# Optimization experiments

Hardware: AMD Instinct MI355X
Metric: run time of the kernel (lower is better)

Reference implementation:

```python
import jax, jax.numpy as jnp
import numpy as np

N = 100000
F_IN = 128
F_OUT = 128
NNZ = 1_600_000  # avg degree 16


def spmm(rows, cols, vals, X, n):
    """Sparse [n,n] (COO: rows, cols, vals) times dense X [n,d] -> [n,d]."""
    return jax.ops.segment_sum(vals[:, None] * X[cols], rows, num_segments=n)


def setup_inputs() -> dict:
    key = jax.random.key(0)
    ks = jax.random.split(key, 8)
    x = jax.random.normal(ks[0], (N, F_IN), dtype=jnp.float32)
    W = jax.random.normal(ks[1], (F_IN, F_OUT), dtype=jnp.float32) * 0.05
    kernel = jnp.ones((N, 1), dtype=jnp.float32)  # tf.ones_initializer
    phi0_rows = jax.random.randint(ks[2], (NNZ,), 0, N, dtype=jnp.int64)
    phi0_cols = jax.random.randint(ks[3], (NNZ,), 0, N, dtype=jnp.int64)
    phi0_vals = jax.random.uniform(ks[4], (NNZ,), dtype=jnp.float32)
    phi1_rows = jax.random.randint(ks[5], (NNZ,), 0, N, dtype=jnp.int64)
    phi1_cols = jax.random.randint(ks[6], (NNZ,), 0, N, dtype=jnp.int64)
    phi1_vals = jax.random.uniform(ks[7], (NNZ,), dtype=jnp.float32)
    return {
        "x": x, "W": W, "kernel": kernel,
        "phi0_rows": phi0_rows, "phi0_cols": phi0_cols, "phi0_vals": phi0_vals,
        "phi1_rows": phi1_rows, "phi1_cols": phi1_cols, "phi1_vals": phi1_vals,
    }


def reference(x, W, kernel, phi0_rows, phi0_cols, phi0_vals,
              phi1_rows, phi1_cols, phi1_vals):
    # X' = x @ W  (dense feature projection)
    X_prime = x @ W  # [N, F_OUT]
    # X'_t = phi0 @ X'  (SpMM with wavelet basis)
    X_t = spmm(phi0_rows, phi0_cols, phi0_vals, X_prime, N)
    # out = phi1 @ (kernel * X'_t)  (elementwise spectral scaling then SpMM)
    out = spmm(phi1_rows, phi1_cols, phi1_vals, kernel * X_t, N)
    return jax.nn.relu(out)
```

## Files before the change

### kernel.cpp

```cpp
#include <hip/hip_runtime.h>


constexpr int kN = 100000;
constexpr int kF = 128;
constexpr int kNNZ = 1600000;

constexpr int kBuckets = (kN + 255) / 256;
constexpr int kBucketCap = 4608;
constexpr int kChunk = 7168;
constexpr int kChunkBlocks = (kNNZ + kChunk - 1) / kChunk;
constexpr int kSlotsPerMat = kChunkBlocks * kChunk;
constexpr int kDirStride = kBuckets + 1;
constexpr int kGemmBlocks = (kN + 63) / 64;
constexpr int kRowBlocks = kN * 32 / 256;
constexpr int kTransBlocks = 64;

typedef short bf16x8 __attribute__((ext_vector_type(8)));
typedef float f32x4 __attribute__((ext_vector_type(4)));
typedef unsigned short ushort4v __attribute__((ext_vector_type(4)));

__device__ __forceinline__ unsigned short f32_to_bf16(float f) {
    unsigned int u = __float_as_uint(f);
    u += 0x7fffu + ((u >> 16) & 1u);
    return (unsigned short)(u >> 16);
}
__device__ __forceinline__ float bf16_to_f32(unsigned short h) {
    return __uint_as_float((unsigned int)h << 16);
}

__global__ __launch_bounds__(256) void scatter_transpose(
    const float* __restrict__ W, unsigned short* __restrict__ Wt,
    const int* __restrict__ r0, const int* __restrict__ c0, const float* __restrict__ v0,
    const int* __restrict__ r1, const int* __restrict__ c1, const float* __restrict__ v1,
    unsigned long long* __restrict__ stg, unsigned short* __restrict__ dir) {
    const int t = threadIdx.x;
    if (blockIdx.x < kTransBlocks) {
        const int e = blockIdx.x * 256 + t;
        const int n = e & 127, k = e >> 7;
        Wt[n * 128 + k] = f32_to_bf16(W[e]);
        return;
    }

    __shared__ unsigned long long recs[kChunk];
    __shared__ int hist[kDirStride];
    __shared__ int cur[kDirStride];
    __shared__ int sc2[256];

    const int b = blockIdx.x - kTransBlocks;
    const bool m1 = b >= kChunkBlocks;
    const int cb = m1 ? b - kChunkBlocks : b;
    const int* rows = m1 ? r1 : r0;
    const int* cols = m1 ? c1 : c0;
    const float* vals = m1 ? v1 : v0;
    unsigned long long* dst = stg + (size_t)b * kChunk;
    unsigned short* dirm = dir + (size_t)b * kDirStride;

    for (int i = t; i < kDirStride; i += 256) hist[i] = 0;
    __syncthreads();

    const int base0 = cb * kChunk;
    const int cnt = min(kNNZ - base0, kChunk);

    for (int j = t; j < cnt; j += 256) atomicAdd(&hist[rows[base0 + j] >> 8], 1);
    __syncthreads();

    int s = 0;
    if (t < 196) s = hist[2 * t] + hist[2 * t + 1];
    sc2[t] = (t < 196) ? s : 0;
    __syncthreads();
    #pragma unroll
    for (int off = 1; off < 256; off <<= 1) {
        const int add = (t >= off) ? sc2[t - off] : 0;
        __syncthreads();
        sc2[t] += add;
        __syncthreads();
    }
    if (t < 196) {
        const int ex = sc2[t] - s;
        cur[2 * t] = ex;
        cur[2 * t + 1] = ex + hist[2 * t];
        dirm[2 * t] = (unsigned short)ex;
        dirm[2 * t + 1] = (unsigned short)(ex + hist[2 * t]);
    }
    __syncthreads();

    for (int j = t; j < cnt; j += 256) {
        const int idx = base0 + j;
        const int r = rows[idx];
        const int bk = r >> 8;
        const int pos = atomicAdd(&cur[bk], 1);
        const unsigned int key = ((unsigned int)(r & 255) << 17) | (unsigned int)cols[idx];
        recs[pos] = ((unsigned long long)__float_as_uint(vals[idx]) << 32) | key;
    }
    __syncthreads();

    for (int j = t; j < cnt; j += 256) dst[j] = recs[j];
}

__global__ __launch_bounds__(256) void gemm_mfma(const float* __restrict__ x,
                                                 const unsigned short* __restrict__ Wt,
                                                 unsigned short* __restrict__ Xpb) {
    __shared__ __align__(16) unsigned short xs[64 * 128];
    const int t = threadIdx.x;
    const int rowBase = blockIdx.x * 64;

    {
        const int lrow = t >> 2;
        const int q = t & 3;
        int srow = rowBase + lrow;
        if (srow >= kN) srow = kN - 1;
        const float4* xr = (const float4*)(x + (size_t)srow * kF) + q * 8;
        #pragma unroll
        for (int i = 0; i < 8; ++i) {
            const float4 f = xr[i];
            ushort4v h;
            h.x = f32_to_bf16(f.x); h.y = f32_to_bf16(f.y);
            h.z = f32_to_bf16(f.z); h.w = f32_to_bf16(f.w);
            const int kidx = q * 32 + i * 4;
            *(ushort4v*)&xs[lrow * 128 + (kidx ^ ((lrow & 7) << 3))] = h;
        }
    }
    __syncthreads();

    const int w = t >> 6;
    const int l = t & 63;
    const int lr = l & 15;
    const int lq = l >> 4;

    f32x4 acc[8];
    #pragma unroll
    for (int n = 0; n < 8; ++n) acc[n] = (f32x4){0.f, 0.f, 0.f, 0.f};

    const int arow = w * 16 + lr;
    #pragma unroll
    for (int ks = 0; ks < 4; ++ks) {
        const int akidx = ks * 32 + lq * 8;
        const bf16x8 a = *(const bf16x8*)&xs[arow * 128 + (akidx ^ ((arow & 7) << 3))];
        #pragma unroll
        for (int n = 0; n < 8; ++n) {
            const int bn = n * 16 + lr;
            const bf16x8 b = *(const bf16x8*)(Wt + bn * 128 + akidx);
            acc[n] = __builtin_amdgcn_mfma_f32_16x16x32_bf16(a, b, acc[n], 0, 0, 0);
        }
    }

    #pragma unroll
    for (int j = 0; j < 4; ++j) {
        const int row = rowBase + w * 16 + lq * 4 + j;
        if (row < kN) {
            unsigned short* orow = Xpb + (size_t)row * kF + lr;
            #pragma unroll
            for (int n = 0; n < 8; ++n) orow[n * 16] = f32_to_bf16(acc[n][j]);
        }
    }
}

__global__ __launch_bounds__(512) void bucket_sort(
    const unsigned long long* __restrict__ stg,
    const unsigned short* __restrict__ dir,
    unsigned long long* __restrict__ sortedG,
    int* __restrict__ rs, int* __restrict__ re) {
    __shared__ unsigned long long sorted[kBucketCap];
    __shared__ int rlen[kChunkBlocks];
    __shared__ int gst[kChunkBlocks];
    __shared__ int hist[256];
    __shared__ int sc[256];
    __shared__ int cur[256];

    const int bidx = blockIdx.x;
    const bool m1 = bidx >= kBuckets;
    const int bk = m1 ? bidx - kBuckets : bidx;
    const int t = threadIdx.x;
    const unsigned long long* stgm = stg + (m1 ? (size_t)kSlotsPerMat : 0);

    if (t < kChunkBlocks) {
        const unsigned short* dd =
            dir + (size_t)((m1 ? kChunkBlocks : 0) + t) * kDirStride;
        const int s = dd[bk];
        rlen[t] = dd[bk + 1] - s;
        gst[t] = t * kChunk + s;
    }
    if (t < 256) hist[t] = 0;
    __syncthreads();

    const int g = t >> 5;
    const int lane = t & 31;

    for (int blk = g; blk < kChunkBlocks; blk += 16) {
        const int len = rlen[blk];
        const int gs = gst[blk];
        for (int i = lane; i < len; i += 32) {
            const unsigned int lo = (unsigned int)stgm[gs + i];
            atomicAdd(&hist[(lo >> 17) & 255], 1);
        }
    }
    __syncthreads();

    const int v = (t < 256) ? hist[t] : 0;
    if (t < 256) sc[t] = v;
    __syncthreads();
    #pragma unroll
    for (int off = 1; off < 256; off <<= 1) {
        const int add = (t < 256 && t >= off) ? sc[t - off] : 0;
        __syncthreads();
        if (t < 256) sc[t] += add;
        __syncthreads();
    }
    if (t < 256) cur[t] = sc[t] - v;
    __syncthreads();

    for (int blk = g; blk < kChunkBlocks; blk += 16) {
        const int len = rlen[blk];
        const int gs = gst[blk];
        for (int i = lane; i < len; i += 32) {
            const unsigned long long p = stgm[gs + i];
            const int lrow = (int)(((unsigned int)p >> 17) & 255);
            sorted[atomicAdd(&cur[lrow], 1)] = p;
        }
    }
    __syncthreads();

    const int nrec = sc[255];
    const size_t outBase = (size_t)bidx * kBucketCap;
    for (int j = t; j < nrec; j += 512) sortedG[outBase + j] = sorted[j];
    if (t < 256) {
        const int row = bk * 256 + t;
        if (row < kN) {
            const int rg = (m1 ? kN : 0) + row;
            rs[rg] = (int)outBase + sc[t] - hist[t];
            re[rg] = (int)outBase + sc[t];
        }
    }
}

template <bool ROW_SCALE, bool RELU, bool OUT_BF16>
__global__ __launch_bounds__(256) void spmm_csr(const int* __restrict__ rs,
                                                const int* __restrict__ re,
                                                const unsigned long long* __restrict__ rec,
                                                const float* __restrict__ scale,
                                                const unsigned short* __restrict__ Xin,
                                                void* __restrict__ Xout) {
    const int tid = blockIdx.x * 256 + threadIdx.x;
    const int r = tid >> 5;
    const int lane = tid & 31;

    const int s = rs[r];
    const int e = re[r];

    float4 acc = make_float4(0.f, 0.f, 0.f, 0.f);

    for (int base = s; base < e; base += 32) {
        int cl = 0;
        float vl = 0.f;
        if (base + lane < e) {
            const unsigned long long p = rec[base + lane];
            cl = (int)((unsigned int)p & 0x1FFFF);
            vl = __uint_as_float((unsigned int)(p >> 32));
        }
        const int m4 = (min(32, e - base) + 3) & ~3;
        for (int j = 0; j < m4; j += 4) {
            const int c0 = __shfl(cl, j, 32);
            const int c1 = __shfl(cl, j + 1, 32);
            const int c2 = __shfl(cl, j + 2, 32);
            const int c3 = __shfl(cl, j + 3, 32);
            const float w0 = __shfl(vl, j, 32);
            const float w1 = __shfl(vl, j + 1, 32);
            const float w2 = __shfl(vl, j + 2, 32);
            const float w3 = __shfl(vl, j + 3, 32);
            const ushort4v x0 = *(const ushort4v*)(Xin + (size_t)c0 * kF + lane * 4);
            const ushort4v x1 = *(const ushort4v*)(Xin + (size_t)c1 * kF + lane * 4);
            const ushort4v x2 = *(const ushort4v*)(Xin + (size_t)c2 * kF + lane * 4);
            const ushort4v x3 = *(const ushort4v*)(Xin + (size_t)c3 * kF + lane * 4);
            acc.x = fmaf(w0, bf16_to_f32(x0.x), acc.x);
            acc.y = fmaf(w0, bf16_to_f32(x0.y), acc.y);
            acc.z = fmaf(w0, bf16_to_f32(x0.z), acc.z);
            acc.w = fmaf(w0, bf16_to_f32(x0.w), acc.w);
            acc.x = fmaf(w1, bf16_to_f32(x1.x), acc.x);
            acc.y = fmaf(w1, bf16_to_f32(x1.y), acc.y);
            acc.z = fmaf(w1, bf16_to_f32(x1.z), acc.z);
            acc.w = fmaf(w1, bf16_to_f32(x1.w), acc.w);
            acc.x = fmaf(w2, bf16_to_f32(x2.x), acc.x);
            acc.y = fmaf(w2, bf16_to_f32(x2.y), acc.y);
            acc.z = fmaf(w2, bf16_to_f32(x2.z), acc.z);
            acc.w = fmaf(w2, bf16_to_f32(x2.w), acc.w);
            acc.x = fmaf(w3, bf16_to_f32(x3.x), acc.x);
            acc.y = fmaf(w3, bf16_to_f32(x3.y), acc.y);
            acc.z = fmaf(w3, bf16_to_f32(x3.z), acc.z);
            acc.w = fmaf(w3, bf16_to_f32(x3.w), acc.w);
        }
    }
    if (ROW_SCALE) {
        const float k = scale[r];
        acc.x *= k; acc.y *= k; acc.z *= k; acc.w *= k;
    }
    if (RELU) {
        acc.x = fmaxf(acc.x, 0.f); acc.y = fmaxf(acc.y, 0.f);
        acc.z = fmaxf(acc.z, 0.f); acc.w = fmaxf(acc.w, 0.f);
    }
    if (OUT_BF16) {
        ushort4v o;
        o.x = f32_to_bf16(acc.x); o.y = f32_to_bf16(acc.y);
        o.z = f32_to_bf16(acc.z); o.w = f32_to_bf16(acc.w);
        *(ushort4v*)((unsigned short*)Xout + (size_t)r * kF + lane * 4) = o;
    } else {
        ((float4*)Xout)[(size_t)r * 32 + lane] = acc;
    }
}

extern "C" void kernel_launch(void* const* d_in, const int* in_sizes, int n_in,
                              void* d_out, int out_size, void* d_ws, size_t ws_size,
                              hipStream_t stream) {
    const float* x    = (const float*)d_in[0];
    const float* W    = (const float*)d_in[1];
    const float* kern = (const float*)d_in[2];
    const int*   p0r  = (const int*)d_in[3];
    const int*   p0c  = (const int*)d_in[4];
    const float* p0v  = (const float*)d_in[5];
    const int*   p1r  = (const int*)d_in[6];
    const int*   p1c  = (const int*)d_in[7];
    const float* p1v  = (const float*)d_in[8];

    unsigned long long* stg = (unsigned long long*)d_out;

    char* w = (char*)d_ws;
    size_t off = 0;
    unsigned short* Xpb = (unsigned short*)(w + off); off += (size_t)kN * kF * 2;
    unsigned short* Xtb = (unsigned short*)(w + off); off += (size_t)kN * kF * 2;
    unsigned short* Wt = (unsigned short*)(w + off);  off += 128 * 128 * 2;
    unsigned short* dir = (unsigned short*)(w + off);
    off += (size_t)2 * kChunkBlocks * kDirStride * 2;
    off = (off + 15) & ~(size_t)15;
    unsigned long long* sortedG = (unsigned long long*)(w + off);
    off += (size_t)2 * kBuckets * kBucketCap * 8;
    int* rs = (int*)(w + off);                        off += (size_t)2 * kN * 4;
    int* re = (int*)(w + off);                        off += (size_t)2 * kN * 4;

    scatter_transpose<<<kTransBlocks + 2 * kChunkBlocks, 256, 0, stream>>>(
        W, Wt, p0r, p0c, p0v, p1r, p1c, p1v, stg, dir);

    gemm_mfma<<<kGemmBlocks, 256, 0, stream>>>(x, Wt, Xpb);

    bucket_sort<<<2 * kBuckets, 512, 0, stream>>>(stg, dir, sortedG, rs, re);

    spmm_csr<true, false, true><<<kRowBlocks, 256, 0, stream>>>(
        rs, re, sortedG, kern, Xpb, Xtb);

    spmm_csr<false, true, false><<<kRowBlocks, 256, 0, stream>>>(
        rs + kN, re + kN, sortedG, nullptr, Xtb, (float*)d_out);
}
```

Before: 214.2 us.

## Merge bucket sort and GEMM into one launch; use nontemporal loads/stores in SpMM

Combines the bucket_sort and gemm_mfma kernels into one launch. Blocks branch by index to do either sorting or a GEMM over a 128-row tile with 512 threads, so the two independent stages can overlap on the GPU and one launch gap goes away. The SpMM kernel now uses nontemporal loads for the edge records and nontemporal stores for its outputs, to avoid polluting the cache that holds the gathered feature rows. The costs are a larger shared-memory footprint per block (a union of both layouts), which may lower occupancy for the GEMM blocks. The nontemporal output of the first SpMM may also hurt reuse when the second SpMM reads it.

```diff
diff --git a/kernel.cpp b/kernel.cpp
--- a/kernel.cpp
+++ b/kernel.cpp
@@ -11,9 +11,10 @@
 constexpr int kChunkBlocks = (kNNZ + kChunk - 1) / kChunk;
 constexpr int kSlotsPerMat = kChunkBlocks * kChunk;
 constexpr int kDirStride = kBuckets + 1;
-constexpr int kGemmBlocks = (kN + 63) / 64;
+constexpr int kTransBlocks = 64;
+constexpr int kSortBlocks = 2 * kBuckets;
+constexpr int kGemmBlocks = (kN + 127) / 128;
 constexpr int kRowBlocks = kN * 32 / 256;
-constexpr int kTransBlocks = 64;
 
 typedef short bf16x8 __attribute__((ext_vector_type(8)));
 typedef float f32x4 __attribute__((ext_vector_type(4)));
@@ -97,138 +98,139 @@
     for (int j = t; j < cnt; j += 256) dst[j] = recs[j];
 }
 
-__global__ __launch_bounds__(256) void gemm_mfma(const float* __restrict__ x,
-                                                 const unsigned short* __restrict__ Wt,
-                                                 unsigned short* __restrict__ Xpb) {
-    __shared__ __align__(16) unsigned short xs[64 * 128];
-    const int t = threadIdx.x;
-    const int rowBase = blockIdx.x * 64;
-
-    {
-        const int lrow = t >> 2;
-        const int q = t & 3;
-        int srow = rowBase + lrow;
-        if (srow >= kN) srow = kN - 1;
-        const float4* xr = (const float4*)(x + (size_t)srow * kF) + q * 8;
-        #pragma unroll
-        for (int i = 0; i < 8; ++i) {
-            const float4 f = xr[i];
-            ushort4v h;
-            h.x = f32_to_bf16(f.x); h.y = f32_to_bf16(f.y);
-            h.z = f32_to_bf16(f.z); h.w = f32_to_bf16(f.w);
-            const int kidx = q * 32 + i * 4;
-            *(ushort4v*)&xs[lrow * 128 + (kidx ^ ((lrow & 7) << 3))] = h;
-        }
-    }
-    __syncthreads();
-
-    const int w = t >> 6;
-    const int l = t & 63;
-    const int lr = l & 15;
-    const int lq = l >> 4;
-
-    f32x4 acc[8];
-    #pragma unroll
-    for (int n = 0; n < 8; ++n) acc[n] = (f32x4){0.f, 0.f, 0.f, 0.f};
-
-    const int arow = w * 16 + lr;
-    #pragma unroll
-    for (int ks = 0; ks < 4; ++ks) {
-        const int akidx = ks * 32 + lq * 8;
-        const bf16x8 a = *(const bf16x8*)&xs[arow * 128 + (akidx ^ ((arow & 7) << 3))];
-        #pragma unroll
-        for (int n = 0; n < 8; ++n) {
-            const int bn = n * 16 + lr;
-            const bf16x8 b = *(const bf16x8*)(Wt + bn * 128 + akidx);
-            acc[n] = __builtin_amdgcn_mfma_f32_16x16x32_bf16(a, b, acc[n], 0, 0, 0);
-        }
-    }
-
-    #pragma unroll
-    for (int j = 0; j < 4; ++j) {
-        const int row = rowBase + w * 16 + lq * 4 + j;
-        if (row < kN) {
-            unsigned short* orow = Xpb + (size_t)row * kF + lr;
-            #pragma unroll
-            for (int n = 0; n < 8; ++n) orow[n * 16] = f32_to_bf16(acc[n][j]);
-        }
-    }
-}
-
-__global__ __launch_bounds__(512) void bucket_sort(
+__global__ __launch_bounds__(512) void sort_gemm(
     const unsigned long long* __restrict__ stg,
     const unsigned short* __restrict__ dir,
     unsigned long long* __restrict__ sortedG,
-    int* __restrict__ rs, int* __restrict__ re) {
-    __shared__ unsigned long long sorted[kBucketCap];
-    __shared__ int rlen[kChunkBlocks];
-    __shared__ int gst[kChunkBlocks];
-    __shared__ int hist[256];
-    __shared__ int sc[256];
-    __shared__ int cur[256];
-
-    const int bidx = blockIdx.x;
-    const bool m1 = bidx >= kBuckets;
-    const int bk = m1 ? bidx - kBuckets : bidx;
+    int* __restrict__ rs, int* __restrict__ re,
+    const float* __restrict__ x, const unsigned short* __restrict__ Wt,
+    unsigned short* __restrict__ Xpb) {
+    __shared__ __align__(16) char smem[41728];
     const int t = threadIdx.x;
-    const unsigned long long* stgm = stg + (m1 ? (size_t)kSlotsPerMat : 0);
-
-    if (t < kChunkBlocks) {
-        const unsigned short* dd =
-            dir + (size_t)((m1 ? kChunkBlocks : 0) + t) * kDirStride;
-        const int s = dd[bk];
-        rlen[t] = dd[bk + 1] - s;
-        gst[t] = t * kChunk + s;
-    }
-    if (t < 256) hist[t] = 0;
-    __syncthreads();
-
-    const int g = t >> 5;
-    const int lane = t & 31;
-
-    for (int blk = g; blk < kChunkBlocks; blk += 16) {
-        const int len = rlen[blk];
-        const int gs = gst[blk];
-        for (int i = lane; i < len; i += 32) {
-            const unsigned int lo = (unsigned int)stgm[gs + i];
-            atomicAdd(&hist[(lo >> 17) & 255], 1);
-        }
-    }
-    __syncthreads();
-
-    const int v = (t < 256) ? hist[t] : 0;
-    if (t < 256) sc[t] = v;
-    __syncthreads();
-    #pragma unroll
-    for (int off = 1; off < 256; off <<= 1) {
-        const int add = (t < 256 && t >= off) ? sc[t - off] : 0;
-        __syncthreads();
-        if (t < 256) sc[t] += add;
-        __syncthreads();
-    }
-    if (t < 256) cur[t] = sc[t] - v;
-    __syncthreads();
-
-    for (int blk = g; blk < kChunkBlocks; blk += 16) {
-        const int len = rlen[blk];
-        const int gs = gst[blk];
-        for (int i = lane; i < len; i += 32) {
-            const unsigned long long p = stgm[gs + i];
-            const int lrow = (int)(((unsigned int)p >> 17) & 255);
-            sorted[atomicAdd(&cur[lrow], 1)] = p;
-        }
-    }
-    __syncthreads();
-
-    const int nrec = sc[255];
-    const size_t outBase = (size_t)bidx * kBucketCap;
-    for (int j = t; j < nrec; j += 512) sortedG[outBase + j] = sorted[j];
-    if (t < 256) {
-        const int row = bk * 256 + t;
-        if (row < kN) {
-            const int rg = (m1 ? kN : 0) + row;
-            rs[rg] = (int)outBase + sc[t] - hist[t];
-            re[rg] = (int)outBase + sc[t];
+
+    if (blockIdx.x < kSortBlocks) {
+        unsigned long long* sorted = (unsigned long long*)smem;
+        int* rlen = (int*)(smem + 36864);
+        int* gst  = (int*)(smem + 36864 + 896);
+        int* hist = (int*)(smem + 36864 + 1792);
+        int* sc   = (int*)(smem + 36864 + 2816);
+        int* cur  = (int*)(smem + 36864 + 3840);
+
+        const int bidx = blockIdx.x;
+        const bool m1 = bidx >= kBuckets;
+        const int bk = m1 ? bidx - kBuckets : bidx;
+        const unsigned long long* stgm = stg + (m1 ? (size_t)kSlotsPerMat : 0);
+
+        if (t < kChunkBlocks) {
+            const unsigned short* dd =
+                dir + (size_t)((m1 ? kChunkBlocks : 0) + t) * kDirStride;
+            const int s = dd[bk];
+            rlen[t] = dd[bk + 1] - s;
+            gst[t] = t * kChunk + s;
+        }
+        if (t < 256) hist[t] = 0;
+        __syncthreads();
+
+        const int g = t >> 5;
+        const int lane = t & 31;
+
+        for (int blk = g; blk < kChunkBlocks; blk += 16) {
+            const int len = rlen[blk];
+            const int gs = gst[blk];
+            for (int i = lane; i < len; i += 32) {
+                const unsigned int lo = (unsigned int)stgm[gs + i];
+                atomicAdd(&hist[(lo >> 17) & 255], 1);
+            }
+        }
+        __syncthreads();
+
+        const int v = (t < 256) ? hist[t] : 0;
+        if (t < 256) sc[t] = v;
+        __syncthreads();
+        #pragma unroll
+        for (int off = 1; off < 256; off <<= 1) {
+            const int add = (t < 256 && t >= off) ? sc[t - off] : 0;
+            __syncthreads();
+            if (t < 256) sc[t] += add;
+            __syncthreads();
+        }
+        if (t < 256) cur[t] = sc[t] - v;
+        __syncthreads();
+
+        for (int blk = g; blk < kChunkBlocks; blk += 16) {
+            const int len = rlen[blk];
+            const int gs = gst[blk];
+            for (int i = lane; i < len; i += 32) {
+                const unsigned long long p = stgm[gs + i];
+                const int lrow = (int)(((unsigned int)p >> 17) & 255);
+                sorted[atomicAdd(&cur[lrow], 1)] = p;
+            }
+        }
+        __syncthreads();
+
+        const int nrec = sc[255];
+        const size_t outBase = (size_t)bidx * kBucketCap;
+        for (int j = t; j < nrec; j += 512) sortedG[outBase + j] = sorted[j];
+        if (t < 256) {
+            const int row = bk * 256 + t;
+            if (row < kN) {
+                const int rg = (m1 ? kN : 0) + row;
+                rs[rg] = (int)outBase + sc[t] - hist[t];
+                re[rg] = (int)outBase + sc[t];
+            }
+        }
+    } else {
+        unsigned short* xs = (unsigned short*)smem;
+        const int rowBase = (blockIdx.x - kSortBlocks) * 128;
+
+        {
+            const int lrow = t >> 2;
+            const int q = t & 3;
+            int srow = rowBase + lrow;
+            if (srow >= kN) srow = kN - 1;
+            const float4* xr = (const float4*)(x + (size_t)srow * kF) + q * 8;
+            #pragma unroll
+            for (int i = 0; i < 8; ++i) {
+                const float4 f = xr[i];
+                ushort4v h;
+                h.x = f32_to_bf16(f.x); h.y = f32_to_bf16(f.y);
+                h.z = f32_to_bf16(f.z); h.w = f32_to_bf16(f.w);
+                const int kidx = q * 32 + i * 4;
+                *(ushort4v*)&xs[lrow * 128 + (kidx ^ ((lrow & 7) << 3))] = h;
+            }
+        }
+        __syncthreads();
+
+        const int w = t >> 6;
+        const int l = t & 63;
+        const int lr = l & 15;
+        const int lq = l >> 4;
+
+        f32x4 acc[8];
+        #pragma unroll
+        for (int n = 0; n < 8; ++n) acc[n] = (f32x4){0.f, 0.f, 0.f, 0.f};
+
+        const int arow = w * 16 + lr;
+        #pragma unroll
+        for (int ks = 0; ks < 4; ++ks) {
+            const int akidx = ks * 32 + lq * 8;
+            const bf16x8 a = *(const bf16x8*)&xs[arow * 128 + (akidx ^ ((arow & 7) << 3))];
+            #pragma unroll
+            for (int n = 0; n < 8; ++n) {
+                const int bn = n * 16 + lr;
+                const bf16x8 b = *(const bf16x8*)(Wt + bn * 128 + akidx);
+                acc[n] = __builtin_amdgcn_mfma_f32_16x16x32_bf16(a, b, acc[n], 0, 0, 0);
+            }
+        }
+
+        #pragma unroll
+        for (int j = 0; j < 4; ++j) {
+            const int row = rowBase + w * 16 + lq * 4 + j;
+            if (row < kN) {
+                unsigned short* orow = Xpb + (size_t)row * kF + lr;
+                #pragma unroll
+                for (int n = 0; n < 8; ++n) orow[n * 16] = f32_to_bf16(acc[n][j]);
+            }
         }
     }
 }
@@ -253,7 +255,7 @@
         int cl = 0;
         float vl = 0.f;
         if (base + lane < e) {
-            const unsigned long long p = rec[base + lane];
+            const unsigned long long p = __builtin_nontemporal_load(&rec[base + lane]);
             cl = (int)((unsigned int)p & 0x1FFFF);
             vl = __uint_as_float((unsigned int)(p >> 32));
         }
@@ -301,9 +303,12 @@
         ushort4v o;
         o.x = f32_to_bf16(acc.x); o.y = f32_to_bf16(acc.y);
         o.z = f32_to_bf16(acc.z); o.w = f32_to_bf16(acc.w);
-        *(ushort4v*)((unsigned short*)Xout + (size_t)r * kF + lane * 4) = o;
+        __builtin_nontemporal_store(
+            o, (ushort4v*)((unsigned short*)Xout + (size_t)r * kF + lane * 4));
     } else {
-        ((float4*)Xout)[(size_t)r * 32 + lane] = acc;
+        f32x4 o;
+        o.x = acc.x; o.y = acc.y; o.z = acc.z; o.w = acc.w;
+        __builtin_nontemporal_store(o, (f32x4*)Xout + (size_t)r * 32 + lane);
     }
 }
 
@@ -338,9 +343,8 @@
     scatter_transpose<<<kTransBlocks + 2 * kChunkBlocks, 256, 0, stream>>>(
         W, Wt, p0r, p0c, p0v, p1r, p1c, p1v, stg, dir);
 
-    gemm_mfma<<<kGemmBlocks, 256, 0, stream>>>(x, Wt, Xpb);
-
-    bucket_sort<<<2 * kBuckets, 512, 0, stream>>>(stg, dir, sortedG, rs, re);
+    sort_gemm<<<kSortBlocks + kGemmBlocks, 512, 0, stream>>>(
+        stg, dir, sortedG, rs, re, x, Wt, Xpb);
 
     spmm_csr<true, false, true><<<kRowBlocks, 256, 0, stream>>>(
         rs, re, sortedG, kern, Xpb, Xtb);
```

After: 207.3 us. 1.03x faster.
